# Kernel optimization log

Hardware: AMD Instinct MI355X
Metric: run time of the kernel (lower is better)

The kernel has to match this reference:

```python
import jax, jax.numpy as jnp
import numpy as np

NUM_EXPERTS = 4

def setup_inputs() -> dict:
    key = jax.random.key(0)
    k = jax.random.split(key, 6)
    B, S, D = 8, 4096, 1024
    H = D * 2  # mlp_ratio = 2
    x = jax.random.normal(k[0], (B, S, D), dtype=jnp.float32)
    expert_mask = jax.random.randint(k[1], (B, S), 0, NUM_EXPERTS, dtype=jnp.int32)
    w1 = jax.random.normal(k[2], (H, D), dtype=jnp.float32) * (D ** -0.5)
    b1 = jax.random.normal(k[3], (H,), dtype=jnp.float32) * 0.02
    w2 = jax.random.normal(k[4], (D, H), dtype=jnp.float32) * (H ** -0.5)
    b2 = jax.random.normal(k[5], (D,), dtype=jnp.float32) * 0.02
    return {"x": x, "expert_mask": expert_mask, "w1": w1, "b1": b1, "w2": w2, "b2": b2}


def reference(x, expert_mask, w1, b1, w2, b2):
    """Nested SwiGLU MLP with token-wise expert-dependent active hidden width.

    Expert e in [0, E) activates the first Hh * 2^(e+1-E) units of each of the
    gate/up branches (Hh = H/2); the largest expert (e = E-1) uses the full width.
    out = (silu(gate) * up masked to active width) @ W2[:, :Hh].T + b2
    """
    E = NUM_EXPERTS
    H = w1.shape[0]
    Hh = H // 2  # per-branch (gate / up) width
    # dense expand: z = x @ W1.T + b1  -> [B, S, H]
    z = jnp.einsum('bsd,hd->bsh', x, w1) + b1
    g = z[..., :Hh]  # gate branch
    u = z[..., Hh:]  # up branch
    # active width per token: Hh // 2^(E-1-e)
    active = Hh // (2 ** (E - 1 - expert_mask))  # [B, S] int
    mask = (jnp.arange(Hh) < active[..., None]).astype(x.dtype)  # [B, S, Hh]
    a = jax.nn.silu(g) * u * mask  # zeros outside the token's nested width
    out = jnp.einsum('bsh,dh->bsd', a, w2[:, :Hh]) + b2
    return out
```

## Files before the change

### kernel.cpp

```cpp
#include <hip/hip_runtime.h>
#include <stdint.h>


typedef __attribute__((ext_vector_type(8))) __bf16 bf16x8;
typedef __attribute__((ext_vector_type(4))) float f32x4;

#define MFMA16(a, b, c) __builtin_amdgcn_mfma_f32_16x16x32_bf16(a, b, c, 0, 0, 0)

#define BAR() do { __builtin_amdgcn_sched_barrier(0); \
                   asm volatile("s_barrier" ::: "memory"); \
                   __builtin_amdgcn_sched_barrier(0); } while (0)
#define VMCNT(n) asm volatile("s_waitcnt vmcnt(" #n ")" ::: "memory")

static __device__ __forceinline__ unsigned short f2bf(float f) {
  union { float f; uint32_t u; } v; v.f = f;
  uint32_t r = v.u + 0x7FFFu + ((v.u >> 16) & 1u);
  return (unsigned short)(r >> 16);
}

static __device__ __forceinline__ void gload_lds16(const void* g, void* l) {
  __builtin_amdgcn_global_load_lds(
      (const __attribute__((address_space(1))) void*)g,
      (__attribute__((address_space(3))) void*)l, 16, 0, 0);
}

__global__ void conv_w1_kernel(const float* __restrict__ w1,
                               unsigned short* __restrict__ w1b) {
  int i = blockIdx.x * 256 + threadIdx.x;
  float4 v = ((const float4*)w1)[i];
  ushort4 o; o.x = f2bf(v.x); o.y = f2bf(v.y); o.z = f2bf(v.z); o.w = f2bf(v.w);
  ((ushort4*)w1b)[i] = o;
}

__global__ void conv_w2_kernel(const float* __restrict__ w2,
                               unsigned short* __restrict__ w2b) {
  int i = blockIdx.x * 256 + threadIdx.x;
  int d = i >> 8;
  int h4 = (i & 255) * 4;
  float4 v = *(const float4*)(w2 + (size_t)d * 2048 + h4);
  ushort4 o; o.x = f2bf(v.x); o.y = f2bf(v.y); o.z = f2bf(v.z); o.w = f2bf(v.w);
  *(ushort4*)(w2b + (size_t)d * 1024 + h4) = o;
}

__global__ void hist_kernel(const int* __restrict__ emask, int* __restrict__ hist) {
  __shared__ int h[4];
  int tid = threadIdx.x;
  if (tid < 4) h[tid] = 0;
  __syncthreads();
  int e = emask[blockIdx.x * 128 + tid];
  atomicAdd(&h[e], 1);
  __syncthreads();
  if (tid < 4) hist[blockIdx.x * 4 + tid] = h[tid];
}

__global__ void scan_kernel(const int* __restrict__ hist, int* __restrict__ off) {
  __shared__ int total[4];
  int tid = threadIdx.x;
  if (tid < 4) {
    int s = 0;
    for (int b = 0; b < 256; ++b) s += hist[b * 4 + tid];
    total[tid] = s;
  }
  __syncthreads();
  if (tid < 4) {
    int base = 0;
    for (int j = 0; j < tid; ++j) base += total[j];
    int run = base;
    for (int b = 0; b < 256; ++b) {
      off[b * 4 + tid] = run;
      run += hist[b * 4 + tid];
    }
  }
}

__global__ void scatter_kernel(const int* __restrict__ emask,
                               const int* __restrict__ off,
                               int* __restrict__ perm, int* __restrict__ em_sorted) {
  __shared__ int c0[4];
  int tid = threadIdx.x;
  int lane = tid & 63, wid = tid >> 6;
  int t = blockIdx.x * 128 + tid;
  int e = emask[t];
  unsigned long long b0 = __ballot(e == 0);
  unsigned long long b1 = __ballot(e == 1);
  unsigned long long b2 = __ballot(e == 2);
  unsigned long long b3 = __ballot(e == 3);
  if (tid == 0) {
    c0[0] = __popcll(b0); c0[1] = __popcll(b1);
    c0[2] = __popcll(b2); c0[3] = __popcll(b3);
  }
  __syncthreads();
  unsigned long long mine = (e == 0) ? b0 : (e == 1) ? b1 : (e == 2) ? b2 : b3;
  int rank = __popcll(mine & ((1ull << lane) - 1ull));
  if (wid) rank += c0[e];
  int pos = off[blockIdx.x * 4 + e] + rank;
  perm[pos] = t;
  em_sorted[pos] = e;
}

__global__ void xconv_kernel(const float* __restrict__ x, const int* __restrict__ perm,
                             unsigned short* __restrict__ xs) {
  int gid = blockIdx.x * 256 + threadIdx.x;
  int s = gid >> 7;
  int seg = gid & 127;
  int tok = perm[s];
  const float* src = x + (size_t)tok * 1024 + seg * 8;
  float4 v0 = *(const float4*)(src);
  float4 v1 = *(const float4*)(src + 4);
  bf16x8 hv;
  hv[0] = (__bf16)v0.x; hv[1] = (__bf16)v0.y; hv[2] = (__bf16)v0.z; hv[3] = (__bf16)v0.w;
  hv[4] = (__bf16)v1.x; hv[5] = (__bf16)v1.y; hv[6] = (__bf16)v1.z; hv[7] = (__bf16)v1.w;
  *(bf16x8*)(xs + (size_t)s * 1024 + seg * 8) = hv;
}

static __device__ __forceinline__ int block_max_e(const int* em_sorted, int m0,
                                                  int tid, int* sred) {
  int v = 0;
  if (tid < 128) v = em_sorted[m0 + tid];
  #pragma unroll
  for (int o = 32; o; o >>= 1) v = max(v, __shfl_xor(v, o));
  if ((tid & 63) == 0) sred[tid >> 6] = v;
  __syncthreads();
  return max(sred[0], sred[1]);
}

__global__ __launch_bounds__(256, 4)
void gemm1_sorted_kernel(const unsigned short* __restrict__ xs,
                         const int* __restrict__ em_sorted,
                         const unsigned short* __restrict__ w1b,
                         const float* __restrict__ b1,
                         unsigned short* __restrict__ a_out) {
  __shared__ __align__(16) char lds[32768];
  __shared__ int sred[4];
  char* AS = lds;
  char* BS = lds + 16384;

  const int tid = threadIdx.x;
  const int lane = tid & 63;
  const int w = tid >> 6;
  const int wm = w & 1;
  const int wn = w >> 1;
  const int m0 = blockIdx.x * 128;
  const int n0 = blockIdx.y * 64;

  int maxe = block_max_e(em_sorted, m0, tid, sred);
  if (n0 >= (128 << maxe)) return;

  f32x4 accg[4][2] = {};
  f32x4 accu[4][2] = {};

  for (int k0 = 0; k0 < 1024; k0 += 64) {
    #pragma unroll
    for (int i = 0; i < 4; ++i) {
      int c = (w * 4 + i) * 64 + lane;
      int p = c * 16;
      int r = p >> 7;
      int kb16 = ((p >> 4) & 7) ^ (r & 7);
      gload_lds16((const char*)xs + (((size_t)(m0 + r) * 1024 + k0) * 2) + kb16 * 16,
                  AS + (w * 4 + i) * 1024);
      int h = (r < 64) ? (n0 + r) : (1024 + n0 + (r - 64));
      gload_lds16((const char*)w1b + (((size_t)h * 1024 + k0) * 2) + kb16 * 16,
                  BS + (w * 4 + i) * 1024);
    }
    __syncthreads();
    #pragma unroll
    for (int kk = 0; kk < 2; ++kk) {
      const int kbyte = kk * 64 + (lane >> 4) * 16;
      bf16x8 af[4], bg[2], bu[2];
      #pragma unroll
      for (int m = 0; m < 4; ++m) {
        int r = wm * 64 + m * 16 + (lane & 15);
        int o = (r * 128 + kbyte) ^ ((r & 7) << 4);
        af[m] = *(const bf16x8*)(AS + o);
      }
      #pragma unroll
      for (int n = 0; n < 2; ++n) {
        int r = wn * 32 + n * 16 + (lane & 15);
        int o = (r * 128 + kbyte) ^ ((r & 7) << 4);
        bg[n] = *(const bf16x8*)(BS + o);
        bu[n] = *(const bf16x8*)(BS + 8192 + o);
      }
      #pragma unroll
      for (int m = 0; m < 4; ++m)
        #pragma unroll
        for (int n = 0; n < 2; ++n) {
          accg[m][n] = MFMA16(af[m], bg[n], accg[m][n]);
          accu[m][n] = MFMA16(af[m], bu[n], accu[m][n]);
        }
    }
    __syncthreads();
  }
  #pragma unroll
  for (int m = 0; m < 4; ++m) {
    int rbase = m0 + wm * 64 + m * 16 + (lane >> 4) * 4;
    int act[4];
    #pragma unroll
    for (int r = 0; r < 4; ++r) act[r] = 128 << em_sorted[rbase + r];
    #pragma unroll
    for (int n = 0; n < 2; ++n) {
      int col = n0 + wn * 32 + n * 16 + (lane & 15);
      float b1g = b1[col], b1u = b1[col + 1024];
      #pragma unroll
      for (int r = 0; r < 4; ++r) {
        float g = accg[m][n][r] + b1g;
        float u = accu[m][n][r] + b1u;
        float s = g / (1.f + __expf(-g));
        float val = (col < act[r]) ? (s * u) : 0.f;
        a_out[(size_t)(rbase + r) * 1024 + col] = f2bf(val);
      }
    }
  }
}

static __device__ __forceinline__ void ds_loadA(const char* Abase, int lane,
                                                bf16x8 (&af)[4][2], int mh) {
  #pragma unroll
  for (int mf = 0; mf < 4; ++mf)
    #pragma unroll
    for (int kk = 0; kk < 2; ++kk) {
      int r = mh * 64 + mf * 16 + (lane & 15);
      int o = (r * 128 + kk * 64 + ((lane >> 4) * 16)) ^ ((r & 7) << 4);
      af[mf][kk] = *(const bf16x8*)(Abase + o);
    }
}

static __device__ __forceinline__ void ds_loadB(const char* Bbase, int lane, int wc,
                                                bf16x8 (&bf)[2][2], int nh) {
  #pragma unroll
  for (int nl = 0; nl < 2; ++nl)
    #pragma unroll
    for (int kk = 0; kk < 2; ++kk) {
      int n = nh * 2 + nl;
      int r = (wc & 1) * 64 + n * 16 + (lane & 15);
      int o = (r * 128 + kk * 64 + ((lane >> 4) * 16)) ^ ((r & 7) << 4);
      bf[nl][kk] = *(const bf16x8*)(Bbase + o);
    }
}

static __device__ __forceinline__ void mfma_quad(bf16x8 (&af)[4][2], bf16x8 (&bf)[2][2],
                                                 f32x4 (&acc)[8][4], int mh, int nh) {
  __builtin_amdgcn_s_setprio(1);
  #pragma unroll
  for (int mf = 0; mf < 4; ++mf)
    #pragma unroll
    for (int nl = 0; nl < 2; ++nl)
      #pragma unroll
      for (int kk = 0; kk < 2; ++kk)
        acc[mh * 4 + mf][nh * 2 + nl] =
            MFMA16(af[mf][kk], bf[nl][kk], acc[mh * 4 + mf][nh * 2 + nl]);
  __builtin_amdgcn_s_setprio(0);
}

template <class ST>
static __device__ __forceinline__ void kpair_steady(const ST& st, char* lds, int j,
    int lane, int wr, int wc, bf16x8 (&af)[4][2], bf16x8 (&bf0)[2][2],
    bf16x8 (&bf1)[2][2], f32x4 (&acc)[8][4]) {
  const int a = 2 * j, b = 2 * j + 1;
  const char* Aa = lds + (a & 1) * 32768 + wr * 16384;
  const char* Ab = lds + (b & 1) * 32768 + wr * 16384;
  const char* Ba = lds + 65536 + (a & 1) * 32768 + (wc >> 1) * 16384;
  const char* Bb = lds + 65536 + (b & 1) * 32768 + (wc >> 1) * 16384;
  ds_loadA(Aa, lane, af, 0); ds_loadB(Ba, lane, wc, bf0, 0);
  st.stageA(b, 0);            BAR(); mfma_quad(af, bf0, acc, 0, 0); BAR();
  ds_loadB(Ba, lane, wc, bf1, 1);
  st.stageA(b, 1);            BAR(); mfma_quad(af, bf1, acc, 0, 1); BAR();
  ds_loadA(Aa, lane, af, 1);
  st.stageB(a + 2, 0);        BAR(); mfma_quad(af, bf0, acc, 1, 0); BAR();
  st.stageB(a + 2, 1); VMCNT(4); BAR(); mfma_quad(af, bf1, acc, 1, 1); BAR();
  ds_loadA(Ab, lane, af, 0); ds_loadB(Bb, lane, wc, bf0, 0);
  st.stageA(a + 2, 0);        BAR(); mfma_quad(af, bf0, acc, 0, 0); BAR();
  ds_loadB(Bb, lane, wc, bf1, 1);
  st.stageA(a + 2, 1);        BAR(); mfma_quad(af, bf1, acc, 0, 1); BAR();
  ds_loadA(Ab, lane, af, 1);
  st.stageB(b + 2, 0);        BAR(); mfma_quad(af, bf0, acc, 1, 0); BAR();
  st.stageB(b + 2, 1); VMCNT(4); BAR(); mfma_quad(af, bf1, acc, 1, 1); BAR();
}

template <class ST>
static __device__ __forceinline__ void kpair_last(const ST& st, char* lds, int j,
    int lane, int wr, int wc, bf16x8 (&af)[4][2], bf16x8 (&bf0)[2][2],
    bf16x8 (&bf1)[2][2], f32x4 (&acc)[8][4]) {
  const int a = 2 * j, b = 2 * j + 1;
  const char* Aa = lds + (a & 1) * 32768 + wr * 16384;
  const char* Ab = lds + (b & 1) * 32768 + wr * 16384;
  const char* Ba = lds + 65536 + (a & 1) * 32768 + (wc >> 1) * 16384;
  const char* Bb = lds + 65536 + (b & 1) * 32768 + (wc >> 1) * 16384;
  ds_loadA(Aa, lane, af, 0); ds_loadB(Ba, lane, wc, bf0, 0);
  st.stageA(b, 0); BAR(); mfma_quad(af, bf0, acc, 0, 0); BAR();
  ds_loadB(Ba, lane, wc, bf1, 1);
  st.stageA(b, 1); BAR(); mfma_quad(af, bf1, acc, 0, 1); BAR();
  ds_loadA(Aa, lane, af, 1);
  BAR(); mfma_quad(af, bf0, acc, 1, 0); BAR();
  VMCNT(0); BAR(); mfma_quad(af, bf1, acc, 1, 1); BAR();
  ds_loadA(Ab, lane, af, 0); ds_loadB(Bb, lane, wc, bf0, 0);
  BAR(); mfma_quad(af, bf0, acc, 0, 0); BAR();
  ds_loadB(Bb, lane, wc, bf1, 1);
  BAR(); mfma_quad(af, bf1, acc, 0, 1); BAR();
  ds_loadA(Ab, lane, af, 1);
  BAR(); mfma_quad(af, bf0, acc, 1, 0); BAR();
  mfma_quad(af, bf1, acc, 1, 1);
}

template <class ST>
static __device__ __forceinline__ void prologue(const ST& st) {
  st.stageA(0, 0); st.stageA(0, 1);
  st.stageB(0, 0); st.stageB(0, 1);
  st.stageB(1, 0); st.stageB(1, 1);
  VMCNT(4); BAR();
}

#define STAGE_DECODE(kb)                         \
  int r = (kb) * 8 + (lane >> 3);                \
  int s = (lane & 7) ^ (r & 7);

struct G2Stage {
  const char* a_in; const char* w2b; char* lds; int m0, n0; int w, lane;
  __device__ __forceinline__ void stageA(int t, int half) const {
    char* dst = lds + (t & 1) * 32768 + half * 16384;
    #pragma unroll
    for (int i = 0; i < 2; ++i) {
      int kb = w * 2 + i;
      STAGE_DECODE(kb)
      gload_lds16(a_in + (size_t)(m0 + half * 128 + r) * 2048 + t * 128 + s * 16,
                  dst + kb * 1024);
    }
  }
  __device__ __forceinline__ void stageB(int t, int half) const {
    char* dst = lds + 65536 + (t & 1) * 32768 + half * 16384;
    #pragma unroll
    for (int i = 0; i < 2; ++i) {
      int kb = w * 2 + i;
      STAGE_DECODE(kb)
      gload_lds16(w2b + (size_t)(n0 + half * 128 + r) * 2048 + t * 128 + s * 16,
                  dst + kb * 1024);
    }
  }
};

__global__ __launch_bounds__(512, 2)
void gemm2_kernel8(const unsigned short* __restrict__ a_in,
                   const int* __restrict__ em_sorted,
                   const int* __restrict__ perm,
                   const unsigned short* __restrict__ w2b,
                   const float* __restrict__ b2, float* __restrict__ out) {
  __shared__ __align__(16) char lds[131072];
  const int tid = threadIdx.x, lane = tid & 63, w = tid >> 6;
  const int wr = w >> 2, wc = w & 3;
  const int m0 = blockIdx.y * 256, n0 = blockIdx.x * 256;

  int v = em_sorted[m0 + (tid & 255)];
  #pragma unroll
  for (int o = 32; o; o >>= 1) v = max(v, __shfl_xor(v, o));
  int* sred = (int*)lds;
  if (lane == 0) sred[w] = v;
  __syncthreads();
  int maxe = sred[0];
  #pragma unroll
  for (int i = 1; i < 8; ++i) maxe = max(maxe, sred[i]);
  __syncthreads();
  const int J = 1 << maxe;

  G2Stage st{(const char*)a_in, (const char*)w2b, lds, m0, n0, w, lane};
  f32x4 acc[8][4] = {};
  bf16x8 af[4][2], bf0[2][2], bf1[2][2];

  prologue(st);
  #pragma clang loop unroll(disable)
  for (int j = 0; j < J - 1; ++j)
    kpair_steady(st, lds, j, lane, wr, wc, af, bf0, bf1, acc);
  kpair_last(st, lds, J - 1, lane, wr, wc, af, bf0, bf1, acc);

  #pragma unroll
  for (int mf = 0; mf < 8; ++mf) {
    int r0 = m0 + wr * 128 + mf * 16 + (lane >> 4) * 4;
    int tok[4];
    #pragma unroll
    for (int rr = 0; rr < 4; ++rr) tok[rr] = perm[r0 + rr];
    #pragma unroll
    for (int nf = 0; nf < 4; ++nf) {
      int col = n0 + wc * 64 + nf * 16 + (lane & 15);
      float bb = b2[col];
      #pragma unroll
      for (int rr = 0; rr < 4; ++rr)
        out[(size_t)tok[rr] * 1024 + col] = acc[mf][nf][rr] + bb;
    }
  }
}

extern "C" void kernel_launch(void* const* d_in, const int* in_sizes, int n_in,
                              void* d_out, int out_size, void* d_ws, size_t ws_size,
                              hipStream_t stream) {
  const float* x  = (const float*)d_in[0];
  const int* em   = (const int*)d_in[1];
  const float* w1 = (const float*)d_in[2];
  const float* b1 = (const float*)d_in[3];
  const float* w2 = (const float*)d_in[4];
  const float* b2 = (const float*)d_in[5];
  float* out = (float*)d_out;

  char* ws = (char*)d_ws;
  unsigned short* a_ws = (unsigned short*)ws;
  unsigned short* w1b  = (unsigned short*)(ws + 67108864);
  unsigned short* w2b  = (unsigned short*)(ws + 71303168);
  unsigned short* xs   = (unsigned short*)(ws + 73400320);
  int* perm      = (int*)(ws + 140509184);
  int* em_sorted = (int*)(ws + 140640256);
  int* hist      = (int*)(ws + 140771328);
  int* off       = (int*)(ws + 140775424);

  conv_w1_kernel<<<2048, 256, 0, stream>>>(w1, w1b);
  conv_w2_kernel<<<1024, 256, 0, stream>>>(w2, w2b);
  hist_kernel<<<256, 128, 0, stream>>>(em, hist);
  scan_kernel<<<1, 64, 0, stream>>>(hist, off);
  scatter_kernel<<<256, 128, 0, stream>>>(em, off, perm, em_sorted);
  xconv_kernel<<<16384, 256, 0, stream>>>(x, perm, xs);
  gemm1_sorted_kernel<<<dim3(256, 16), 256, 0, stream>>>(xs, em_sorted, w1b, b1, a_ws);
  gemm2_kernel8<<<dim3(4, 128), 512, 0, stream>>>(a_ws, em_sorted, perm, w2b, b2, out);
}
```

Before: 214.4 us.

## Stage GEMM2 epilogue through swizzled LDS and reverse row-tile dispatch order

The GEMM2 epilogue now writes accumulators into LDS, using an XOR swizzle to avoid bank conflicts, in two half-tile passes. Each wave then reads back whole 256-column rows and scatters them to the permuted token rows with float4 stores, replacing scalar strided 4-byte stores. Row tiles are also dispatched in reverse order, so the heaviest experts (sorted last) are scheduled first to even out load imbalance. The cost is extra barriers and LDS round trips in the epilogue.

Result: faster. 201.0 us (-6.2%).

```diff
diff --git a/kernel.cpp b/kernel.cpp
--- a/kernel.cpp
+++ b/kernel.cpp
@@ -346,7 +346,7 @@
   __shared__ __align__(16) char lds[131072];
   const int tid = threadIdx.x, lane = tid & 63, w = tid >> 6;
   const int wr = w >> 2, wc = w & 3;
-  const int m0 = blockIdx.y * 256, n0 = blockIdx.x * 256;
+  const int m0 = (127 - blockIdx.y) * 256, n0 = blockIdx.x * 256;
 
   int v = em_sorted[m0 + (tid & 255)];
   #pragma unroll
@@ -371,18 +371,32 @@
   kpair_last(st, lds, J - 1, lane, wr, wc, af, bf0, bf1, acc);
 
   #pragma unroll
-  for (int mf = 0; mf < 8; ++mf) {
-    int r0 = m0 + wr * 128 + mf * 16 + (lane >> 4) * 4;
-    int tok[4];
-    #pragma unroll
-    for (int rr = 0; rr < 4; ++rr) tok[rr] = perm[r0 + rr];
-    #pragma unroll
-    for (int nf = 0; nf < 4; ++nf) {
-      int col = n0 + wc * 64 + nf * 16 + (lane & 15);
-      float bb = b2[col];
-      #pragma unroll
-      for (int rr = 0; rr < 4; ++rr)
-        out[(size_t)tok[rr] * 1024 + col] = acc[mf][nf][rr] + bb;
+  for (int p = 0; p < 2; ++p) {
+    __syncthreads();
+    if (wr == p) {
+      #pragma unroll
+      for (int mf = 0; mf < 8; ++mf)
+        #pragma unroll
+        for (int nf = 0; nf < 4; ++nf) {
+          int col = wc * 64 + nf * 16 + (lane & 15);
+          #pragma unroll
+          for (int rr = 0; rr < 4; ++rr) {
+            int rl = mf * 16 + (lane >> 4) * 4 + rr;
+            int byte = (rl * 1024 + col * 4) ^ (((rl >> 2) & 3) << 6);
+            *(float*)(lds + byte) = acc[mf][nf][rr];
+          }
+        }
+    }
+    __syncthreads();
+    float4 bb = *(const float4*)(b2 + n0 + lane * 4);
+    #pragma unroll
+    for (int i = 0; i < 16; ++i) {
+      int rl = i * 8 + w;
+      int tok = perm[m0 + p * 128 + rl];
+      int byte = (rl * 1024 + lane * 16) ^ (((rl >> 2) & 3) << 6);
+      float4 vv = *(const float4*)(lds + byte);
+      vv.x += bb.x; vv.y += bb.y; vv.z += bb.z; vv.w += bb.w;
+      *(float4*)(out + (size_t)tok * 1024 + n0 + lane * 4) = vv;
     }
   }
 }
```
